# Performance work log

Measured on AMD Instinct MI355X. Metric: run time of the kernel, lower is better.

Reference implementation:

```python
import jax, jax.numpy as jnp
import numpy as np

N_NODES = 100000
IN_CH, HID_CH, OUT_CH = 128, 128, 64
N_EDGES = 1600000


def _gcn_conv(x, W, b, src, dst, num_nodes):
    """PyG GCNConv with gcn_norm(add_self_loops=True): adds one self-loop per
    node to the given edge set, symmetric deg^-1/2 normalization, then
    gather-scale-scatter of the linearly transformed features."""
    loop = jnp.arange(num_nodes)
    s = jnp.concatenate([src, loop])
    d = jnp.concatenate([dst, loop])
    # degree over targets (flow source_to_target), edge weights = 1
    deg = jax.ops.segment_sum(jnp.ones_like(s, x.dtype), d, num_segments=num_nodes)
    dinv = jnp.where(deg > 0, deg ** -0.5, 0.0)
    norm = dinv[s] * dinv[d]                      # [E']
    h = x @ W                                     # [N, out]
    msg = h[s] * norm[:, None]                    # [E', out] gather + scale
    out = jax.ops.segment_sum(msg, d, num_segments=num_nodes)  # scatter-add
    return out + b


def setup_inputs() -> dict:
    key = jax.random.key(0)
    k = jax.random.split(key, 6)
    x = jax.random.normal(k[0], (N_NODES, IN_CH), dtype=jnp.float32)
    edge_index = jax.random.randint(k[1], (2, N_EDGES), 0, N_NODES, dtype=jnp.int64)
    # Glorot-scale params
    W1 = jax.random.normal(k[2], (IN_CH, HID_CH), dtype=jnp.float32) * (2.0 / (IN_CH + HID_CH)) ** 0.5
    b1 = jnp.zeros((HID_CH,), dtype=jnp.float32)
    W2 = jax.random.normal(k[3], (HID_CH, OUT_CH), dtype=jnp.float32) * (2.0 / (HID_CH + OUT_CH)) ** 0.5
    b2 = jnp.zeros((OUT_CH,), dtype=jnp.float32)
    return {"x": x, "edge_index": edge_index, "W1": W1, "b1": b1, "W2": W2, "b2": b2}


def reference(x, edge_index, W1, b1, W2, b2):
    num_nodes = x.shape[0]
    loop = jnp.arange(num_nodes, dtype=edge_index.dtype)
    # wrapper-level add_self_loops (GCNConv adds another internally)
    src = jnp.concatenate([edge_index[0], loop])
    dst = jnp.concatenate([edge_index[1], loop])
    h = _gcn_conv(x, W1, b1, src, dst, num_nodes)
    h = jax.nn.relu(h)
    h = _gcn_conv(h, W2, b2, src, dst, num_nodes)
    return jax.nn.log_softmax(h, axis=1)
```

## Files before the change

### kernel.cpp

```cpp
#include <hip/hip_runtime.h>
#include <cstdint>
#include <cstddef>

#define IN_CH 128
#define HID_CH 128
#define OUT_CH 64
#define BSH 8
#define PB 4096

typedef unsigned int uint32;
typedef unsigned char uchar;
typedef short bf16x8 __attribute__((ext_vector_type(8)));
typedef float f32x4 __attribute__((ext_vector_type(4)));
typedef float f32x2 __attribute__((ext_vector_type(2)));

static __device__ __forceinline__ unsigned short f2bf(float f) {
    uint32 u = __float_as_uint(f);
    u += 0x7fffu + ((u >> 16) & 1u);
    return (unsigned short)(u >> 16);
}

typedef const __attribute__((address_space(1))) char gch;
typedef __attribute__((address_space(3))) char lch;
static __device__ __forceinline__ void gload16(const void* g, void* l) {
    __builtin_amdgcn_global_load_lds((gch*)g, (lch*)l, 16, 0, 0);
}


__global__ __launch_bounds__(256) void bhist_wtrans(
    const int* __restrict__ dst, int* __restrict__ bcnt, int E, int NB, int gP,
    const float* __restrict__ W1, const float* __restrict__ W2,
    unsigned short* __restrict__ W1t, unsigned short* __restrict__ W2t) {
    if (blockIdx.x >= (uint32)gP) {
        int t = (blockIdx.x - gP) * 256 + threadIdx.x;
        if (t < 128 * 128) {
            int nc = t >> 7, k = t & 127;
            W1t[t] = f2bf(W1[k * 128 + nc]);
        }
        int u = t - 128 * 128;
        if (u >= 0 && u < 64 * 128) {
            int nc = u >> 7, k = u & 127;
            W2t[u] = f2bf(W2[k * 64 + nc]);
        }
        return;
    }
    __shared__ int h[512];
    int t = threadIdx.x;
    int e0 = blockIdx.x * PB;
    int cnt = min(PB, E - e0);
    for (int b = t; b < NB; b += 256) h[b] = 0;
    __syncthreads();
    for (int i = t; i < cnt; i += 256)
        atomicAdd(&h[dst[e0 + i] >> BSH], 1);
    __syncthreads();
    for (int b = t; b < NB; b += 256)
        if (h[b]) atomicAdd(&bcnt[b], h[b]);
}

__global__ void bscan(const int* __restrict__ bcnt, int* __restrict__ bbase,
                      int* __restrict__ bcur, int NB, int E) {
    __shared__ int s[512];
    int t = threadIdx.x;
    int v = (t < NB) ? bcnt[t] : 0;
    s[t] = v;
    __syncthreads();
    for (int o = 1; o < 512; o <<= 1) {
        int add = (t >= o) ? s[t - o] : 0;
        __syncthreads();
        s[t] += add;
        __syncthreads();
    }
    if (t < NB) { bbase[t] = s[t] - v; bcur[t] = 0; }
    if (t == 0) bbase[NB] = E;
}

__global__ __launch_bounds__(256) void part1(
    const int* __restrict__ src, const int* __restrict__ dst,
    const int* __restrict__ bbase, int* __restrict__ bcur,
    int2* __restrict__ pairBuf, int E, int NB) {
    __shared__ int2 pairs[PB];
    __shared__ int hist[512];
    __shared__ int base[512];
    int t = threadIdx.x;
    int e0 = blockIdx.x * PB;
    int cnt = min(PB, E - e0);
    for (int b = t; b < NB; b += 256) hist[b] = 0;
    __syncthreads();
    for (int i = t; i < cnt; i += 256) {
        int s = src[e0 + i], d = dst[e0 + i];
        pairs[i] = make_int2(s, d);
        atomicAdd(&hist[d >> BSH], 1);
    }
    __syncthreads();
    for (int b = t; b < NB; b += 256) {
        int h = hist[b];
        int gb = (h > 0) ? atomicAdd(&bcur[b], h) : 0;
        base[b] = bbase[b] + gb;
        hist[b] = 0;
    }
    __syncthreads();
    for (int i = t; i < cnt; i += 256) {
        int2 p = pairs[i];
        int b = p.y >> BSH;
        int q = base[b] + atomicAdd(&hist[b], 1);
        pairBuf[q] = p;
    }
}

__global__ __launch_bounds__(256) void bucket_build(
    const int2* __restrict__ pairBuf, const int* __restrict__ bbase,
    int* __restrict__ rowptr, int* __restrict__ deg, float* __restrict__ dinv,
    int* __restrict__ csr, int N) {
    __shared__ int cnt[256];
    __shared__ int loc[256];
    int b = blockIdx.x, t = threadIdx.x;
    int start = bbase[b], end = bbase[b + 1];
    cnt[t] = 0;
    __syncthreads();
    for (int i = start + t; i < end; i += 256)
        atomicAdd(&cnt[pairBuf[i].y & 255], 1);
    __syncthreads();
    int v = cnt[t];
    loc[t] = v;
    __syncthreads();
    for (int o = 1; o < 256; o <<= 1) {
        int add = (t >= o) ? loc[t - o] : 0;
        __syncthreads();
        loc[t] += add;
        __syncthreads();
    }
    int excl = loc[t] - v;
    int node = (b << BSH) + t;
    if (node < N) {
        rowptr[node] = start + excl;
        deg[node] = v;
        dinv[node] = rsqrtf((float)(v + 2));
    }
    __syncthreads();
    cnt[t] = excl;
    __syncthreads();
    for (int i = start + t; i < end; i += 256) {
        int2 p = pairBuf[i];
        int q = start + atomicAdd(&cnt[p.y & 255], 1);
        csr[q] = p.x;
    }
}


__global__ __launch_bounds__(256) void gemm1_mfma(
    const float* __restrict__ A, const unsigned short* __restrict__ Wt,
    const float* __restrict__ dinv, uchar* __restrict__ C, int n, int nTiles) {
    constexpr int NT = 8;
    __shared__ unsigned short Ws[128 * 136];
    __shared__ char As[64 * 512];

    const int t = threadIdx.x;

    for (int i = t; i < 128 * 16; i += 256) {
        int rr = i >> 4, sq = i & 15;
        *(uint4*)&Ws[rr * 136 + sq * 8] = *(const uint4*)(Wt + rr * 128 + sq * 8);
    }

    const int w = t >> 6, l = t & 63;
    const int q = l >> 4, r16 = l & 15;
    const int rw = w * 16 + r16;

    for (int tile = blockIdx.x; tile < nTiles; tile += gridDim.x) {
        const int row0 = tile * 64;

#pragma unroll
        for (int rnd = 0; rnd < 8; rnd++) {
            int p = rnd * 4096 + t * 16;
            int row = row0 + (p >> 9);
            int col = p & 511;
            gload16((const char*)A + (size_t)min(row, n - 1) * 512 + col, As + p);
        }
        __syncthreads();

        f32x4 acc[NT];
#pragma unroll
        for (int i = 0; i < NT; i++) acc[i] = (f32x4){0.f, 0.f, 0.f, 0.f};

#pragma unroll
        for (int s = 0; s < 4; s++) {
            const int k0 = s * 32 + q * 8;
            const float* Arow = (const float*)(As + rw * 512);
            float4 v0 = *(const float4*)(Arow + k0);
            float4 v1 = *(const float4*)(Arow + k0 + 4);
            bf16x8 xf;
            xf[0] = (short)f2bf(v0.x); xf[1] = (short)f2bf(v0.y);
            xf[2] = (short)f2bf(v0.z); xf[3] = (short)f2bf(v0.w);
            xf[4] = (short)f2bf(v1.x); xf[5] = (short)f2bf(v1.y);
            xf[6] = (short)f2bf(v1.z); xf[7] = (short)f2bf(v1.w);
#pragma unroll
            for (int nt = 0; nt < NT; nt++) {
                bf16x8 wf = *(const bf16x8*)&Ws[(nt * 16 + r16) * 136 + k0];
                acc[nt] = __builtin_amdgcn_mfma_f32_16x16x32_bf16(wf, xf, acc[nt], 0, 0, 0);
            }
        }

        const int node = row0 + rw;
        const bool nv = node < n;
        const float dv = dinv[min(node, n - 1)];
        uchar* Crow = C + (size_t)node * 128;
#pragma unroll
        for (int nt = 0; nt < NT; nt++) {
            int pk = 0;
            pk = __builtin_amdgcn_cvt_pk_fp8_f32(acc[nt][0] * dv, acc[nt][1] * dv, pk, false);
            pk = __builtin_amdgcn_cvt_pk_fp8_f32(acc[nt][2] * dv, acc[nt][3] * dv, pk, true);
            if (nv) *(uint32*)(Crow + nt * 16 + q * 4) = (uint32)pk;
        }
        __syncthreads();
    }
}


__global__ __launch_bounds__(256) void agg1_fused(
    const uchar* __restrict__ H, const int* __restrict__ csr,
    const int* __restrict__ rowptr, const int* __restrict__ deg,
    const float* __restrict__ dinv, const float* __restrict__ bias,
    const unsigned short* __restrict__ W2t, uchar* __restrict__ H2, int n) {
    __shared__ unsigned short tile[16 * 136];
    int t = threadIdx.x;
    int g = t >> 4;
    int v = blockIdx.x * 16 + g;
    int hl = t & 15;
    int gsel = t & 48;
    bool valid = v < n;
    int vc = valid ? v : 0;
    int base = rowptr[vc];
    int cnt = valid ? deg[vc] : 0;
    const uint32 co = (uint32)(hl * 8);

    f32x2 A0 = (f32x2){0.f, 0.f}, A1 = A0, A2 = A0, A3 = A0;
    f32x2 B0 = A0, B1 = A0, B2 = A0, B3 = A0;

#define ACC128(h, s0, s1, s2, s3)                                   \
    {                                                               \
        s0 += __builtin_amdgcn_cvt_pk_f32_fp8((h).x, false);        \
        s1 += __builtin_amdgcn_cvt_pk_f32_fp8((h).x, true);         \
        s2 += __builtin_amdgcn_cvt_pk_f32_fp8((h).y, false);        \
        s3 += __builtin_amdgcn_cvt_pk_f32_fp8((h).y, true);         \
    }

    for (int j0 = 0; j0 < cnt; j0 += 16) {
        int nj = min(16, cnt - j0);
        int ul = 0;
        if (hl < nj) ul = csr[base + j0 + hl];
        int j = 0;
        for (; j + 8 <= nj; j += 8) {
            int u0 = __shfl(ul, (j + 0) | gsel), u1 = __shfl(ul, (j + 1) | gsel);
            int u2 = __shfl(ul, (j + 2) | gsel), u3 = __shfl(ul, (j + 3) | gsel);
            int u4 = __shfl(ul, (j + 4) | gsel), u5 = __shfl(ul, (j + 5) | gsel);
            int u6 = __shfl(ul, (j + 6) | gsel), u7 = __shfl(ul, (j + 7) | gsel);
            uint2 h0 = *(const uint2*)(H + (((uint32)u0 << 7) + co));
            uint2 h1 = *(const uint2*)(H + (((uint32)u1 << 7) + co));
            uint2 h2 = *(const uint2*)(H + (((uint32)u2 << 7) + co));
            uint2 h3 = *(const uint2*)(H + (((uint32)u3 << 7) + co));
            uint2 h4 = *(const uint2*)(H + (((uint32)u4 << 7) + co));
            uint2 h5 = *(const uint2*)(H + (((uint32)u5 << 7) + co));
            uint2 h6 = *(const uint2*)(H + (((uint32)u6 << 7) + co));
            uint2 h7 = *(const uint2*)(H + (((uint32)u7 << 7) + co));
            ACC128(h0, A0, A1, A2, A3);
            ACC128(h1, B0, B1, B2, B3);
            ACC128(h2, A0, A1, A2, A3);
            ACC128(h3, B0, B1, B2, B3);
            ACC128(h4, A0, A1, A2, A3);
            ACC128(h5, B0, B1, B2, B3);
            ACC128(h6, A0, A1, A2, A3);
            ACC128(h7, B0, B1, B2, B3);
        }
        for (; j + 4 <= nj; j += 4) {
            int u0 = __shfl(ul, (j + 0) | gsel), u1 = __shfl(ul, (j + 1) | gsel);
            int u2 = __shfl(ul, (j + 2) | gsel), u3 = __shfl(ul, (j + 3) | gsel);
            uint2 h0 = *(const uint2*)(H + (((uint32)u0 << 7) + co));
            uint2 h1 = *(const uint2*)(H + (((uint32)u1 << 7) + co));
            uint2 h2 = *(const uint2*)(H + (((uint32)u2 << 7) + co));
            uint2 h3 = *(const uint2*)(H + (((uint32)u3 << 7) + co));
            ACC128(h0, A0, A1, A2, A3);
            ACC128(h1, B0, B1, B2, B3);
            ACC128(h2, A0, A1, A2, A3);
            ACC128(h3, B0, B1, B2, B3);
        }
        for (; j < nj; j++) {
            int u = __shfl(ul, j | gsel);
            uint2 h = *(const uint2*)(H + (((uint32)u << 7) + co));
            ACC128(h, A0, A1, A2, A3);
        }
    }
#undef ACC128

    uint4 pk = make_uint4(0, 0, 0, 0);
    if (valid) {
        float dv = dinv[vc];
        uint2 hv = *(const uint2*)(H + (((uint32)vc << 7) + co));
        f32x2 s0 = __builtin_amdgcn_cvt_pk_f32_fp8(hv.x, false);
        f32x2 s1 = __builtin_amdgcn_cvt_pk_f32_fp8(hv.x, true);
        f32x2 s2 = __builtin_amdgcn_cvt_pk_f32_fp8(hv.y, false);
        f32x2 s3 = __builtin_amdgcn_cvt_pk_f32_fp8(hv.y, true);
        const f32x2* bp = (const f32x2*)(bias + hl * 8);
        f32x2 e0 = dv * ((A0 + B0) + 2.f * s0) + bp[0];
        f32x2 e1 = dv * ((A1 + B1) + 2.f * s1) + bp[1];
        f32x2 e2 = dv * ((A2 + B2) + 2.f * s2) + bp[2];
        f32x2 e3 = dv * ((A3 + B3) + 2.f * s3) + bp[3];
        float o0 = fmaxf(e0[0], 0.f), o1 = fmaxf(e0[1], 0.f);
        float o2 = fmaxf(e1[0], 0.f), o3 = fmaxf(e1[1], 0.f);
        float o4 = fmaxf(e2[0], 0.f), o5 = fmaxf(e2[1], 0.f);
        float o6 = fmaxf(e3[0], 0.f), o7 = fmaxf(e3[1], 0.f);
        pk.x = (uint32)f2bf(o0) | ((uint32)f2bf(o1) << 16);
        pk.y = (uint32)f2bf(o2) | ((uint32)f2bf(o3) << 16);
        pk.z = (uint32)f2bf(o4) | ((uint32)f2bf(o5) << 16);
        pk.w = (uint32)f2bf(o6) | ((uint32)f2bf(o7) << 16);
    }
    *(uint4*)&tile[g * 136 + hl * 8] = pk;
    __syncthreads();

    const int w = t >> 6, l = t & 63;
    const int q = l >> 4, r16 = l & 15;
    f32x4 acc2 = (f32x4){0.f, 0.f, 0.f, 0.f};
#pragma unroll
    for (int s = 0; s < 4; s++) {
        const int k0 = s * 32 + q * 8;
        bf16x8 hf = *(const bf16x8*)&tile[r16 * 136 + k0];
        bf16x8 wf = *(const bf16x8*)(W2t + (size_t)(w * 16 + r16) * 128 + k0);
        acc2 = __builtin_amdgcn_mfma_f32_16x16x32_bf16(wf, hf, acc2, 0, 0, 0);
    }
    const int node = blockIdx.x * 16 + r16;
    if (node < n) {
        const float dv2 = dinv[node];
        int pk2 = 0;
        pk2 = __builtin_amdgcn_cvt_pk_fp8_f32(acc2[0] * dv2, acc2[1] * dv2, pk2, false);
        pk2 = __builtin_amdgcn_cvt_pk_fp8_f32(acc2[2] * dv2, acc2[3] * dv2, pk2, true);
        *(uint32*)(H2 + (size_t)node * 64 + w * 16 + q * 4) = (uint32)pk2;
    }
}

__global__ __launch_bounds__(256) void agg_lsm_64(
    const uchar* __restrict__ H, const int* __restrict__ csr,
    const int* __restrict__ rowptr, const int* __restrict__ deg,
    const float* __restrict__ dinv, const float* __restrict__ bias,
    float* __restrict__ out, int n) {
    int v = blockIdx.x * 16 + (threadIdx.x >> 4);
    int hl = threadIdx.x & 15;
    int gsel = threadIdx.x & 48;
    bool valid = v < n;
    int vc = valid ? v : 0;
    int base = rowptr[vc];
    int cnt = valid ? deg[vc] : 0;
    const uint32 co = (uint32)(hl * 4);

    f32x2 A0 = (f32x2){0.f, 0.f}, A1 = A0, B0 = A0, B1 = A0;

#define ACC64(h, s0, s1)                                            \
    {                                                               \
        s0 += __builtin_amdgcn_cvt_pk_f32_fp8((h), false);          \
        s1 += __builtin_amdgcn_cvt_pk_f32_fp8((h), true);           \
    }

    for (int j0 = 0; j0 < cnt; j0 += 16) {
        int nj = min(16, cnt - j0);
        int ul = 0;
        if (hl < nj) ul = csr[base + j0 + hl];
        int j = 0;
        for (; j + 8 <= nj; j += 8) {
            int u0 = __shfl(ul, (j + 0) | gsel), u1 = __shfl(ul, (j + 1) | gsel);
            int u2 = __shfl(ul, (j + 2) | gsel), u3 = __shfl(ul, (j + 3) | gsel);
            int u4 = __shfl(ul, (j + 4) | gsel), u5 = __shfl(ul, (j + 5) | gsel);
            int u6 = __shfl(ul, (j + 6) | gsel), u7 = __shfl(ul, (j + 7) | gsel);
            uint32 h0 = *(const uint32*)(H + (((uint32)u0 << 6) + co));
            uint32 h1 = *(const uint32*)(H + (((uint32)u1 << 6) + co));
            uint32 h2 = *(const uint32*)(H + (((uint32)u2 << 6) + co));
            uint32 h3 = *(const uint32*)(H + (((uint32)u3 << 6) + co));
            uint32 h4 = *(const uint32*)(H + (((uint32)u4 << 6) + co));
            uint32 h5 = *(const uint32*)(H + (((uint32)u5 << 6) + co));
            uint32 h6 = *(const uint32*)(H + (((uint32)u6 << 6) + co));
            uint32 h7 = *(const uint32*)(H + (((uint32)u7 << 6) + co));
            ACC64(h0, A0, A1);
            ACC64(h1, B0, B1);
            ACC64(h2, A0, A1);
            ACC64(h3, B0, B1);
            ACC64(h4, A0, A1);
            ACC64(h5, B0, B1);
            ACC64(h6, A0, A1);
            ACC64(h7, B0, B1);
        }
        for (; j + 4 <= nj; j += 4) {
            int u0 = __shfl(ul, (j + 0) | gsel), u1 = __shfl(ul, (j + 1) | gsel);
            int u2 = __shfl(ul, (j + 2) | gsel), u3 = __shfl(ul, (j + 3) | gsel);
            uint32 h0 = *(const uint32*)(H + (((uint32)u0 << 6) + co));
            uint32 h1 = *(const uint32*)(H + (((uint32)u1 << 6) + co));
            uint32 h2 = *(const uint32*)(H + (((uint32)u2 << 6) + co));
            uint32 h3 = *(const uint32*)(H + (((uint32)u3 << 6) + co));
            ACC64(h0, A0, A1);
            ACC64(h1, B0, B1);
            ACC64(h2, A0, A1);
            ACC64(h3, B0, B1);
        }
        for (; j < nj; j++) {
            int u = __shfl(ul, j | gsel);
            uint32 h = *(const uint32*)(H + (((uint32)u << 6) + co));
            ACC64(h, A0, A1);
        }
    }
#undef ACC64

    float dv = dinv[vc];
    uint32 hv = *(const uint32*)(H + (((uint32)vc << 6) + co));
    f32x2 s0 = __builtin_amdgcn_cvt_pk_f32_fp8(hv, false);
    f32x2 s1 = __builtin_amdgcn_cvt_pk_f32_fp8(hv, true);
    const f32x2* bp = (const f32x2*)(bias + hl * 4);
    f32x2 w0 = dv * ((A0 + B0) + 2.f * s0) + bp[0];
    f32x2 w1 = dv * ((A1 + B1) + 2.f * s1) + bp[1];
    float v0 = w0[0], v1 = w0[1], v2 = w1[0], v3 = w1[1];
    float m = fmaxf(fmaxf(v0, v1), fmaxf(v2, v3));
    for (int o = 8; o > 0; o >>= 1) m = fmaxf(m, __shfl_xor(m, o));
    float e = (__expf(v0 - m) + __expf(v1 - m)) + (__expf(v2 - m) + __expf(v3 - m));
    for (int o = 8; o > 0; o >>= 1) e += __shfl_xor(e, o);
    float ls = m + __logf(e);
    if (valid)
        *(float4*)(out + (size_t)vc * 64 + hl * 4) =
            make_float4(v0 - ls, v1 - ls, v2 - ls, v3 - ls);
}


extern "C" void kernel_launch(void* const* d_in, const int* in_sizes, int n_in,
                              void* d_out, int out_size, void* d_ws, size_t ws_size,
                              hipStream_t stream) {
    const float* x  = (const float*)d_in[0];
    const int*   ei = (const int*)d_in[1];
    const float* W1 = (const float*)d_in[2];
    const float* b1 = (const float*)d_in[3];
    const float* W2 = (const float*)d_in[4];
    const float* b2 = (const float*)d_in[5];
    float* out = (float*)d_out;

    const int N = in_sizes[0] / IN_CH;
    const int E = in_sizes[1] / 2;
    const int* src = ei;
    const int* dst = ei + E;
    const int NB = (N + 255) >> BSH;

    char* w = (char*)d_ws;
    size_t off = 0;
    auto alloc = [&](size_t bytes) -> char* {
        char* p = w + off;
        off = (off + bytes + 255) & ~(size_t)255;
        return p;
    };
    int*   deg    = (int*)alloc((size_t)N * 4);
    int*   rowptr = (int*)alloc((size_t)N * 4);
    int*   bcnt   = (int*)alloc(512 * 4);
    int*   bbase  = (int*)alloc(513 * 4);
    int*   bcur   = (int*)alloc(512 * 4);
    float* dinv   = (float*)alloc((size_t)N * 4 + 1024);
    int*   csr    = (int*)alloc((size_t)E * 4);
    unsigned short* W1t = (unsigned short*)alloc(128 * 128 * 2);
    unsigned short* W2t = (unsigned short*)alloc(64 * 128 * 2);
    uchar* H1  = (uchar*)alloc((size_t)N * HID_CH);
    char*  scratch = alloc((size_t)E * 8);
    uchar* H2  = (uchar*)scratch;
    int2*  pairBuf = (int2*)scratch;

    hipMemsetAsync(bcnt, 0, 512 * 4, stream);

    int gP = (E + PB - 1) / PB;

    bhist_wtrans<<<gP + 96, 256, 0, stream>>>(dst, bcnt, E, NB, gP, W1, W2, W1t, W2t);
    bscan<<<1, 512, 0, stream>>>(bcnt, bbase, bcur, NB, E);
    part1<<<gP, 256, 0, stream>>>(src, dst, bbase, bcur, pairBuf, E, NB);
    bucket_build<<<NB, 256, 0, stream>>>(pairBuf, bbase, rowptr, deg, dinv, csr, N);

    const int nTiles = (N + 63) / 64;
    const int gG = min(nTiles, 512);
    gemm1_mfma<<<gG, 256, 0, stream>>>(x, W1t, dinv, H1, N, nTiles);
    agg1_fused<<<(N + 15) / 16, 256, 0, stream>>>(H1, csr, rowptr, deg, dinv, b1, W2t, H2, N);
    agg_lsm_64<<<(N + 15) / 16, 256, 0, stream>>>(H2, csr, rowptr, deg, dinv, b2, out, N);
}
```

Before: 242.4 us.

## Widen gather loads to 16 bytes and split neighbors across lane subgroups

Both aggregation kernels now gather 16-byte chunks of fp8 feature rows per lane instead of 8 or 4 bytes. The lanes of a node group are split into subgroups that process different neighbors in parallel, and the partial sums are combined with xor shuffles afterward. The first kernel also preloads its W2 fragments into registers before the gather loop. The goal is fewer, wider memory instructions for the latency-bound gather. The cost is extra shuffle reductions, more accumulator registers and a more complex tail handling.

```diff
diff --git a/kernel.cpp b/kernel.cpp
--- a/kernel.cpp
+++ b/kernel.cpp
@@ -230,17 +230,29 @@
     int vc = valid ? v : 0;
     int base = rowptr[vc];
     int cnt = valid ? deg[vc] : 0;
-    const uint32 co = (uint32)(hl * 8);
-
-    f32x2 A0 = (f32x2){0.f, 0.f}, A1 = A0, A2 = A0, A3 = A0;
-    f32x2 B0 = A0, B1 = A0, B2 = A0, B3 = A0;
-
-#define ACC128(h, s0, s1, s2, s3)                                   \
+    const int par = hl >> 3;
+    const uint32 co16 = (uint32)((hl & 7) * 16);
+
+    const int w = t >> 6, l = t & 63;
+    const int q = l >> 4, r16 = l & 15;
+    bf16x8 wf[4];
+#pragma unroll
+    for (int s = 0; s < 4; s++)
+        wf[s] = *(const bf16x8*)(W2t + (size_t)(w * 16 + r16) * 128 + s * 32 + q * 8);
+
+    f32x2 S0 = (f32x2){0.f, 0.f}, S1 = S0, S2 = S0, S3 = S0;
+    f32x2 S4 = S0, S5 = S0, S6 = S0, S7 = S0;
+
+#define ACCU4(h)                                                    \
     {                                                               \
-        s0 += __builtin_amdgcn_cvt_pk_f32_fp8((h).x, false);        \
-        s1 += __builtin_amdgcn_cvt_pk_f32_fp8((h).x, true);         \
-        s2 += __builtin_amdgcn_cvt_pk_f32_fp8((h).y, false);        \
-        s3 += __builtin_amdgcn_cvt_pk_f32_fp8((h).y, true);         \
+        S0 += __builtin_amdgcn_cvt_pk_f32_fp8((h).x, false);        \
+        S1 += __builtin_amdgcn_cvt_pk_f32_fp8((h).x, true);         \
+        S2 += __builtin_amdgcn_cvt_pk_f32_fp8((h).y, false);        \
+        S3 += __builtin_amdgcn_cvt_pk_f32_fp8((h).y, true);         \
+        S4 += __builtin_amdgcn_cvt_pk_f32_fp8((h).z, false);        \
+        S5 += __builtin_amdgcn_cvt_pk_f32_fp8((h).z, true);         \
+        S6 += __builtin_amdgcn_cvt_pk_f32_fp8((h).w, false);        \
+        S7 += __builtin_amdgcn_cvt_pk_f32_fp8((h).w, true);         \
     }
 
     for (int j0 = 0; j0 < cnt; j0 += 16) {
@@ -248,61 +260,60 @@
         int ul = 0;
         if (hl < nj) ul = csr[base + j0 + hl];
         int j = 0;
-        for (; j + 8 <= nj; j += 8) {
-            int u0 = __shfl(ul, (j + 0) | gsel), u1 = __shfl(ul, (j + 1) | gsel);
-            int u2 = __shfl(ul, (j + 2) | gsel), u3 = __shfl(ul, (j + 3) | gsel);
-            int u4 = __shfl(ul, (j + 4) | gsel), u5 = __shfl(ul, (j + 5) | gsel);
-            int u6 = __shfl(ul, (j + 6) | gsel), u7 = __shfl(ul, (j + 7) | gsel);
-            uint2 h0 = *(const uint2*)(H + (((uint32)u0 << 7) + co));
-            uint2 h1 = *(const uint2*)(H + (((uint32)u1 << 7) + co));
-            uint2 h2 = *(const uint2*)(H + (((uint32)u2 << 7) + co));
-            uint2 h3 = *(const uint2*)(H + (((uint32)u3 << 7) + co));
-            uint2 h4 = *(const uint2*)(H + (((uint32)u4 << 7) + co));
-            uint2 h5 = *(const uint2*)(H + (((uint32)u5 << 7) + co));
-            uint2 h6 = *(const uint2*)(H + (((uint32)u6 << 7) + co));
-            uint2 h7 = *(const uint2*)(H + (((uint32)u7 << 7) + co));
-            ACC128(h0, A0, A1, A2, A3);
-            ACC128(h1, B0, B1, B2, B3);
-            ACC128(h2, A0, A1, A2, A3);
-            ACC128(h3, B0, B1, B2, B3);
-            ACC128(h4, A0, A1, A2, A3);
-            ACC128(h5, B0, B1, B2, B3);
-            ACC128(h6, A0, A1, A2, A3);
-            ACC128(h7, B0, B1, B2, B3);
-        }
-        for (; j + 4 <= nj; j += 4) {
-            int u0 = __shfl(ul, (j + 0) | gsel), u1 = __shfl(ul, (j + 1) | gsel);
-            int u2 = __shfl(ul, (j + 2) | gsel), u3 = __shfl(ul, (j + 3) | gsel);
-            uint2 h0 = *(const uint2*)(H + (((uint32)u0 << 7) + co));
-            uint2 h1 = *(const uint2*)(H + (((uint32)u1 << 7) + co));
-            uint2 h2 = *(const uint2*)(H + (((uint32)u2 << 7) + co));
-            uint2 h3 = *(const uint2*)(H + (((uint32)u3 << 7) + co));
-            ACC128(h0, A0, A1, A2, A3);
-            ACC128(h1, B0, B1, B2, B3);
-            ACC128(h2, A0, A1, A2, A3);
-            ACC128(h3, B0, B1, B2, B3);
-        }
-        for (; j < nj; j++) {
+        for (; j + 16 <= nj; j += 16) {
+            int u0 = __shfl(ul, (j + 0 + par) | gsel);
+            int u1 = __shfl(ul, (j + 2 + par) | gsel);
+            int u2 = __shfl(ul, (j + 4 + par) | gsel);
+            int u3 = __shfl(ul, (j + 6 + par) | gsel);
+            int u4 = __shfl(ul, (j + 8 + par) | gsel);
+            int u5 = __shfl(ul, (j + 10 + par) | gsel);
+            int u6 = __shfl(ul, (j + 12 + par) | gsel);
+            int u7 = __shfl(ul, (j + 14 + par) | gsel);
+            uint4 h0 = *(const uint4*)(H + (((uint32)u0 << 7) + co16));
+            uint4 h1 = *(const uint4*)(H + (((uint32)u1 << 7) + co16));
+            uint4 h2 = *(const uint4*)(H + (((uint32)u2 << 7) + co16));
+            uint4 h3 = *(const uint4*)(H + (((uint32)u3 << 7) + co16));
+            uint4 h4 = *(const uint4*)(H + (((uint32)u4 << 7) + co16));
+            uint4 h5 = *(const uint4*)(H + (((uint32)u5 << 7) + co16));
+            uint4 h6 = *(const uint4*)(H + (((uint32)u6 << 7) + co16));
+            uint4 h7 = *(const uint4*)(H + (((uint32)u7 << 7) + co16));
+            ACCU4(h0); ACCU4(h1); ACCU4(h2); ACCU4(h3);
+            ACCU4(h4); ACCU4(h5); ACCU4(h6); ACCU4(h7);
+        }
+        for (; j + 2 <= nj; j += 2) {
+            int u = __shfl(ul, (j + par) | gsel);
+            uint4 h = *(const uint4*)(H + (((uint32)u << 7) + co16));
+            ACCU4(h);
+        }
+        if (j < nj) {
             int u = __shfl(ul, j | gsel);
-            uint2 h = *(const uint2*)(H + (((uint32)u << 7) + co));
-            ACC128(h, A0, A1, A2, A3);
-        }
-    }
-#undef ACC128
+            if (par == 0) {
+                uint4 h = *(const uint4*)(H + (((uint32)u << 7) + co16));
+                ACCU4(h);
+            }
+        }
+    }
+#undef ACCU4
+
+#define CMB8(S) { f32x2 T_; T_[0] = __shfl_xor(S[0], 8); T_[1] = __shfl_xor(S[1], 8); S += T_; }
+    CMB8(S0); CMB8(S1); CMB8(S2); CMB8(S3); CMB8(S4); CMB8(S5); CMB8(S6); CMB8(S7);
+#undef CMB8
 
     uint4 pk = make_uint4(0, 0, 0, 0);
     if (valid) {
         float dv = dinv[vc];
-        uint2 hv = *(const uint2*)(H + (((uint32)vc << 7) + co));
+        uint2 hv = *(const uint2*)(H + (((uint32)vc << 7) + co16 + (uint32)(par * 8)));
         f32x2 s0 = __builtin_amdgcn_cvt_pk_f32_fp8(hv.x, false);
         f32x2 s1 = __builtin_amdgcn_cvt_pk_f32_fp8(hv.x, true);
         f32x2 s2 = __builtin_amdgcn_cvt_pk_f32_fp8(hv.y, false);
         f32x2 s3 = __builtin_amdgcn_cvt_pk_f32_fp8(hv.y, true);
-        const f32x2* bp = (const f32x2*)(bias + hl * 8);
-        f32x2 e0 = dv * ((A0 + B0) + 2.f * s0) + bp[0];
-        f32x2 e1 = dv * ((A1 + B1) + 2.f * s1) + bp[1];
-        f32x2 e2 = dv * ((A2 + B2) + 2.f * s2) + bp[2];
-        f32x2 e3 = dv * ((A3 + B3) + 2.f * s3) + bp[3];
+        const f32x2* bp = (const f32x2*)(bias + (hl & 7) * 16 + par * 8);
+        f32x2 a0 = par ? S4 : S0, a1 = par ? S5 : S1;
+        f32x2 a2 = par ? S6 : S2, a3 = par ? S7 : S3;
+        f32x2 e0 = dv * (a0 + 2.f * s0) + bp[0];
+        f32x2 e1 = dv * (a1 + 2.f * s1) + bp[1];
+        f32x2 e2 = dv * (a2 + 2.f * s2) + bp[2];
+        f32x2 e3 = dv * (a3 + 2.f * s3) + bp[3];
         float o0 = fmaxf(e0[0], 0.f), o1 = fmaxf(e0[1], 0.f);
         float o2 = fmaxf(e1[0], 0.f), o3 = fmaxf(e1[1], 0.f);
         float o4 = fmaxf(e2[0], 0.f), o5 = fmaxf(e2[1], 0.f);
@@ -312,18 +323,14 @@
         pk.z = (uint32)f2bf(o4) | ((uint32)f2bf(o5) << 16);
         pk.w = (uint32)f2bf(o6) | ((uint32)f2bf(o7) << 16);
     }
-    *(uint4*)&tile[g * 136 + hl * 8] = pk;
-    __syncthreads();
-
-    const int w = t >> 6, l = t & 63;
-    const int q = l >> 4, r16 = l & 15;
+    *(uint4*)&tile[g * 136 + (hl & 7) * 16 + par * 8] = pk;
+    __syncthreads();
+
     f32x4 acc2 = (f32x4){0.f, 0.f, 0.f, 0.f};
 #pragma unroll
     for (int s = 0; s < 4; s++) {
-        const int k0 = s * 32 + q * 8;
-        bf16x8 hf = *(const bf16x8*)&tile[r16 * 136 + k0];
-        bf16x8 wf = *(const bf16x8*)(W2t + (size_t)(w * 16 + r16) * 128 + k0);
-        acc2 = __builtin_amdgcn_mfma_f32_16x16x32_bf16(wf, hf, acc2, 0, 0, 0);
+        bf16x8 hf = *(const bf16x8*)&tile[r16 * 136 + s * 32 + q * 8];
+        acc2 = __builtin_amdgcn_mfma_f32_16x16x32_bf16(wf[s], hf, acc2, 0, 0, 0);
     }
     const int node = blockIdx.x * 16 + r16;
     if (node < n) {
@@ -340,21 +347,30 @@
     const int* __restrict__ rowptr, const int* __restrict__ deg,
     const float* __restrict__ dinv, const float* __restrict__ bias,
     float* __restrict__ out, int n) {
-    int v = blockIdx.x * 16 + (threadIdx.x >> 4);
-    int hl = threadIdx.x & 15;
-    int gsel = threadIdx.x & 48;
+    int t = threadIdx.x;
+    int v = blockIdx.x * 16 + (t >> 4);
+    int hl = t & 15;
+    int gsel = t & 48;
     bool valid = v < n;
     int vc = valid ? v : 0;
     int base = rowptr[vc];
     int cnt = valid ? deg[vc] : 0;
-    const uint32 co = (uint32)(hl * 4);
-
-    f32x2 A0 = (f32x2){0.f, 0.f}, A1 = A0, B0 = A0, B1 = A0;
-
-#define ACC64(h, s0, s1)                                            \
+    const int par4 = hl >> 2;
+    const uint32 co16 = (uint32)((hl & 3) * 16);
+
+    f32x2 S0 = (f32x2){0.f, 0.f}, S1 = S0, S2 = S0, S3 = S0;
+    f32x2 S4 = S0, S5 = S0, S6 = S0, S7 = S0;
+
+#define ACCU4(h)                                                    \
     {                                                               \
-        s0 += __builtin_amdgcn_cvt_pk_f32_fp8((h), false);          \
-        s1 += __builtin_amdgcn_cvt_pk_f32_fp8((h), true);           \
+        S0 += __builtin_amdgcn_cvt_pk_f32_fp8((h).x, false);        \
+        S1 += __builtin_amdgcn_cvt_pk_f32_fp8((h).x, true);         \
+        S2 += __builtin_amdgcn_cvt_pk_f32_fp8((h).y, false);        \
+        S3 += __builtin_amdgcn_cvt_pk_f32_fp8((h).y, true);         \
+        S4 += __builtin_amdgcn_cvt_pk_f32_fp8((h).z, false);        \
+        S5 += __builtin_amdgcn_cvt_pk_f32_fp8((h).z, true);         \
+        S6 += __builtin_amdgcn_cvt_pk_f32_fp8((h).w, false);        \
+        S7 += __builtin_amdgcn_cvt_pk_f32_fp8((h).w, true);         \
     }
 
     for (int j0 = 0; j0 < cnt; j0 += 16) {
@@ -362,55 +378,51 @@
         int ul = 0;
         if (hl < nj) ul = csr[base + j0 + hl];
         int j = 0;
-        for (; j + 8 <= nj; j += 8) {
-            int u0 = __shfl(ul, (j + 0) | gsel), u1 = __shfl(ul, (j + 1) | gsel);
-            int u2 = __shfl(ul, (j + 2) | gsel), u3 = __shfl(ul, (j + 3) | gsel);
-            int u4 = __shfl(ul, (j + 4) | gsel), u5 = __shfl(ul, (j + 5) | gsel);
-            int u6 = __shfl(ul, (j + 6) | gsel), u7 = __shfl(ul, (j + 7) | gsel);
-            uint32 h0 = *(const uint32*)(H + (((uint32)u0 << 6) + co));
-            uint32 h1 = *(const uint32*)(H + (((uint32)u1 << 6) + co));
-            uint32 h2 = *(const uint32*)(H + (((uint32)u2 << 6) + co));
-            uint32 h3 = *(const uint32*)(H + (((uint32)u3 << 6) + co));
-            uint32 h4 = *(const uint32*)(H + (((uint32)u4 << 6) + co));
-            uint32 h5 = *(const uint32*)(H + (((uint32)u5 << 6) + co));
-            uint32 h6 = *(const uint32*)(H + (((uint32)u6 << 6) + co));
-            uint32 h7 = *(const uint32*)(H + (((uint32)u7 << 6) + co));
-            ACC64(h0, A0, A1);
-            ACC64(h1, B0, B1);
-            ACC64(h2, A0, A1);
-            ACC64(h3, B0, B1);
-            ACC64(h4, A0, A1);
-            ACC64(h5, B0, B1);
-            ACC64(h6, A0, A1);
-            ACC64(h7, B0, B1);
+        for (; j + 16 <= nj; j += 16) {
+            int u0 = __shfl(ul, (j + 0 + par4) | gsel);
+            int u1 = __shfl(ul, (j + 4 + par4) | gsel);
+            int u2 = __shfl(ul, (j + 8 + par4) | gsel);
+            int u3 = __shfl(ul, (j + 12 + par4) | gsel);
+            uint4 h0 = *(const uint4*)(H + (((uint32)u0 << 6) + co16));
+            uint4 h1 = *(const uint4*)(H + (((uint32)u1 << 6) + co16));
+            uint4 h2 = *(const uint4*)(H + (((uint32)u2 << 6) + co16));
+            uint4 h3 = *(const uint4*)(H + (((uint32)u3 << 6) + co16));
+            ACCU4(h0); ACCU4(h1); ACCU4(h2); ACCU4(h3);
         }
         for (; j + 4 <= nj; j += 4) {
-            int u0 = __shfl(ul, (j + 0) | gsel), u1 = __shfl(ul, (j + 1) | gsel);
-            int u2 = __shfl(ul, (j + 2) | gsel), u3 = __shfl(ul, (j + 3) | gsel);
-            uint32 h0 = *(const uint32*)(H + (((uint32)u0 << 6) + co));
-            uint32 h1 = *(const uint32*)(H + (((uint32)u1 << 6) + co));
-            uint32 h2 = *(const uint32*)(H + (((uint32)u2 << 6) + co));
-            uint32 h3 = *(const uint32*)(H + (((uint32)u3 << 6) + co));
-            ACC64(h0, A0, A1);
-            ACC64(h1, B0, B1);
-            ACC64(h2, A0, A1);
-            ACC64(h3, B0, B1);
-        }
-        for (; j < nj; j++) {
-            int u = __shfl(ul, j | gsel);
-            uint32 h = *(const uint32*)(H + (((uint32)u << 6) + co));
-            ACC64(h, A0, A1);
-        }
-    }
-#undef ACC64
+            int u = __shfl(ul, (j + par4) | gsel);
+            uint4 h = *(const uint4*)(H + (((uint32)u << 6) + co16));
+            ACCU4(h);
+        }
+        int rem = nj - j;
+        if (rem) {
+            int u = __shfl(ul, ((j + par4) & 15) | gsel);
+            if (par4 < rem) {
+                uint4 h = *(const uint4*)(H + (((uint32)u << 6) + co16));
+                ACCU4(h);
+            }
+        }
+    }
+#undef ACCU4
+
+#define CMB(S, M) { f32x2 T_; T_[0] = __shfl_xor(S[0], M); T_[1] = __shfl_xor(S[1], M); S += T_; }
+    CMB(S0, 4); CMB(S1, 4); CMB(S2, 4); CMB(S3, 4);
+    CMB(S4, 4); CMB(S5, 4); CMB(S6, 4); CMB(S7, 4);
+    CMB(S0, 8); CMB(S1, 8); CMB(S2, 8); CMB(S3, 8);
+    CMB(S4, 8); CMB(S5, 8); CMB(S6, 8); CMB(S7, 8);
+#undef CMB
+
+    f32x2 a0 = (par4 == 0) ? S0 : (par4 == 1) ? S2 : (par4 == 2) ? S4 : S6;
+    f32x2 a1 = (par4 == 0) ? S1 : (par4 == 1) ? S3 : (par4 == 2) ? S5 : S7;
+    const uint32 off = co16 + (uint32)(par4 * 4);
 
     float dv = dinv[vc];
-    uint32 hv = *(const uint32*)(H + (((uint32)vc << 6) + co));
+    uint32 hv = *(const uint32*)(H + (((uint32)vc << 6) + off));
     f32x2 s0 = __builtin_amdgcn_cvt_pk_f32_fp8(hv, false);
     f32x2 s1 = __builtin_amdgcn_cvt_pk_f32_fp8(hv, true);
-    const f32x2* bp = (const f32x2*)(bias + hl * 4);
-    f32x2 w0 = dv * ((A0 + B0) + 2.f * s0) + bp[0];
-    f32x2 w1 = dv * ((A1 + B1) + 2.f * s1) + bp[1];
+    const f32x2* bp = (const f32x2*)(bias + off);
+    f32x2 w0 = dv * (a0 + 2.f * s0) + bp[0];
+    f32x2 w1 = dv * (a1 + 2.f * s1) + bp[1];
     float v0 = w0[0], v1 = w0[1], v2 = w1[0], v3 = w1[1];
     float m = fmaxf(fmaxf(v0, v1), fmaxf(v2, v3));
     for (int o = 8; o > 0; o >>= 1) m = fmaxf(m, __shfl_xor(m, o));
@@ -418,7 +430,7 @@
     for (int o = 8; o > 0; o >>= 1) e += __shfl_xor(e, o);
     float ls = m + __logf(e);
     if (valid)
-        *(float4*)(out + (size_t)vc * 64 + hl * 4) =
+        *(float4*)(out + (size_t)vc * 64 + off) =
             make_float4(v0 - ls, v1 - ls, v2 - ls, v3 - ls);
 }
 
```

Measured after the change: 263.7 us. 1.09x slower.

## Stage neighbor row gathers through LDS with direct 16-byte global-to-LDS loads

Applied to the files above, without the earlier changes.

Both aggregation kernels now fetch neighbor feature rows with 16-byte direct global-to-LDS loads (gload16) into a per-wave staging buffer. Each lane then reads its slice back from LDS and accumulates. The aim is wider, more coalesced gather transactions and fewer small per-lane global loads. In exchange it adds LDS usage (32KB and 16KB per block), which may cut occupancy. It also waits on all loads per 16-edge chunk and always issues loads for 16 edges, even when fewer are valid.

```diff
diff --git a/kernel.cpp b/kernel.cpp
--- a/kernel.cpp
+++ b/kernel.cpp
@@ -220,17 +220,19 @@
     const int* __restrict__ rowptr, const int* __restrict__ deg,
     const float* __restrict__ dinv, const float* __restrict__ bias,
     const unsigned short* __restrict__ W2t, uchar* __restrict__ H2, int n) {
+    __shared__ char stage[4][8192];
     __shared__ unsigned short tile[16 * 136];
     int t = threadIdx.x;
-    int g = t >> 4;
-    int v = blockIdx.x * 16 + g;
+    int slot = t >> 4;
+    int v = blockIdx.x * 16 + slot;
     int hl = t & 15;
     int gsel = t & 48;
+    int w = t >> 6;
+    int gg = (t >> 4) & 3;
     bool valid = v < n;
     int vc = valid ? v : 0;
     int base = rowptr[vc];
     int cnt = valid ? deg[vc] : 0;
-    const uint32 co = (uint32)(hl * 8);
 
     f32x2 A0 = (f32x2){0.f, 0.f}, A1 = A0, A2 = A0, A3 = A0;
     f32x2 B0 = A0, B1 = A0, B2 = A0, B3 = A0;
@@ -243,53 +245,34 @@
         s3 += __builtin_amdgcn_cvt_pk_f32_fp8((h).y, true);         \
     }
 
+    char* sl = stage[w];
+    const char* rg = sl + gg * 256 + hl * 8;
+
     for (int j0 = 0; j0 < cnt; j0 += 16) {
         int nj = min(16, cnt - j0);
         int ul = 0;
         if (hl < nj) ul = csr[base + j0 + hl];
-        int j = 0;
-        for (; j + 8 <= nj; j += 8) {
-            int u0 = __shfl(ul, (j + 0) | gsel), u1 = __shfl(ul, (j + 1) | gsel);
-            int u2 = __shfl(ul, (j + 2) | gsel), u3 = __shfl(ul, (j + 3) | gsel);
-            int u4 = __shfl(ul, (j + 4) | gsel), u5 = __shfl(ul, (j + 5) | gsel);
-            int u6 = __shfl(ul, (j + 6) | gsel), u7 = __shfl(ul, (j + 7) | gsel);
-            uint2 h0 = *(const uint2*)(H + (((uint32)u0 << 7) + co));
-            uint2 h1 = *(const uint2*)(H + (((uint32)u1 << 7) + co));
-            uint2 h2 = *(const uint2*)(H + (((uint32)u2 << 7) + co));
-            uint2 h3 = *(const uint2*)(H + (((uint32)u3 << 7) + co));
-            uint2 h4 = *(const uint2*)(H + (((uint32)u4 << 7) + co));
-            uint2 h5 = *(const uint2*)(H + (((uint32)u5 << 7) + co));
-            uint2 h6 = *(const uint2*)(H + (((uint32)u6 << 7) + co));
-            uint2 h7 = *(const uint2*)(H + (((uint32)u7 << 7) + co));
-            ACC128(h0, A0, A1, A2, A3);
-            ACC128(h1, B0, B1, B2, B3);
-            ACC128(h2, A0, A1, A2, A3);
-            ACC128(h3, B0, B1, B2, B3);
-            ACC128(h4, A0, A1, A2, A3);
-            ACC128(h5, B0, B1, B2, B3);
-            ACC128(h6, A0, A1, A2, A3);
-            ACC128(h7, B0, B1, B2, B3);
-        }
-        for (; j + 4 <= nj; j += 4) {
-            int u0 = __shfl(ul, (j + 0) | gsel), u1 = __shfl(ul, (j + 1) | gsel);
-            int u2 = __shfl(ul, (j + 2) | gsel), u3 = __shfl(ul, (j + 3) | gsel);
-            uint2 h0 = *(const uint2*)(H + (((uint32)u0 << 7) + co));
-            uint2 h1 = *(const uint2*)(H + (((uint32)u1 << 7) + co));
-            uint2 h2 = *(const uint2*)(H + (((uint32)u2 << 7) + co));
-            uint2 h3 = *(const uint2*)(H + (((uint32)u3 << 7) + co));
-            ACC128(h0, A0, A1, A2, A3);
-            ACC128(h1, B0, B1, B2, B3);
-            ACC128(h2, A0, A1, A2, A3);
-            ACC128(h3, B0, B1, B2, B3);
-        }
-        for (; j < nj; j++) {
+#pragma unroll
+        for (int i = 0; i < 8; i++) {
+            int j = i * 2 + (hl >> 3);
             int u = __shfl(ul, j | gsel);
-            uint2 h = *(const uint2*)(H + (((uint32)u << 7) + co));
-            ACC128(h, A0, A1, A2, A3);
+            gload16(H + (((uint32)u << 7) + ((uint32)(hl & 7) << 4)),
+                    sl + i * 1024);
+        }
+        asm volatile("s_waitcnt vmcnt(0)" ::: "memory");
+        __builtin_amdgcn_sched_barrier(0);
+#pragma unroll
+        for (int j = 0; j < 16; j++) {
+            if (j < nj) {
+                uint2 h = *(const uint2*)(rg + (j >> 1) * 1024 + (j & 1) * 128);
+                if (j & 1) { ACC128(h, B0, B1, B2, B3); }
+                else       { ACC128(h, A0, A1, A2, A3); }
+            }
         }
     }
 #undef ACC128
 
+    const uint32 co = (uint32)(hl * 8);
     uint4 pk = make_uint4(0, 0, 0, 0);
     if (valid) {
         float dv = dinv[vc];
@@ -312,10 +295,10 @@
         pk.z = (uint32)f2bf(o4) | ((uint32)f2bf(o5) << 16);
         pk.w = (uint32)f2bf(o6) | ((uint32)f2bf(o7) << 16);
     }
-    *(uint4*)&tile[g * 136 + hl * 8] = pk;
-    __syncthreads();
-
-    const int w = t >> 6, l = t & 63;
+    *(uint4*)&tile[slot * 136 + hl * 8] = pk;
+    __syncthreads();
+
+    const int l = t & 63;
     const int q = l >> 4, r16 = l & 15;
     f32x4 acc2 = (f32x4){0.f, 0.f, 0.f, 0.f};
 #pragma unroll
@@ -340,9 +323,13 @@
     const int* __restrict__ rowptr, const int* __restrict__ deg,
     const float* __restrict__ dinv, const float* __restrict__ bias,
     float* __restrict__ out, int n) {
-    int v = blockIdx.x * 16 + (threadIdx.x >> 4);
-    int hl = threadIdx.x & 15;
-    int gsel = threadIdx.x & 48;
+    __shared__ char stage[4][4096];
+    int t = threadIdx.x;
+    int v = blockIdx.x * 16 + (t >> 4);
+    int hl = t & 15;
+    int gsel = t & 48;
+    int w = t >> 6;
+    int gg = (t >> 4) & 3;
     bool valid = v < n;
     int vc = valid ? v : 0;
     int base = rowptr[vc];
@@ -357,49 +344,29 @@
         s1 += __builtin_amdgcn_cvt_pk_f32_fp8((h), true);           \
     }
 
+    char* sl = stage[w];
+    const char* rg = sl + gg * 256 + hl * 4;
+
     for (int j0 = 0; j0 < cnt; j0 += 16) {
         int nj = min(16, cnt - j0);
         int ul = 0;
         if (hl < nj) ul = csr[base + j0 + hl];
-        int j = 0;
-        for (; j + 8 <= nj; j += 8) {
-            int u0 = __shfl(ul, (j + 0) | gsel), u1 = __shfl(ul, (j + 1) | gsel);
-            int u2 = __shfl(ul, (j + 2) | gsel), u3 = __shfl(ul, (j + 3) | gsel);
-            int u4 = __shfl(ul, (j + 4) | gsel), u5 = __shfl(ul, (j + 5) | gsel);
-            int u6 = __shfl(ul, (j + 6) | gsel), u7 = __shfl(ul, (j + 7) | gsel);
-            uint32 h0 = *(const uint32*)(H + (((uint32)u0 << 6) + co));
-            uint32 h1 = *(const uint32*)(H + (((uint32)u1 << 6) + co));
-            uint32 h2 = *(const uint32*)(H + (((uint32)u2 << 6) + co));
-            uint32 h3 = *(const uint32*)(H + (((uint32)u3 << 6) + co));
-            uint32 h4 = *(const uint32*)(H + (((uint32)u4 << 6) + co));
-            uint32 h5 = *(const uint32*)(H + (((uint32)u5 << 6) + co));
-            uint32 h6 = *(const uint32*)(H + (((uint32)u6 << 6) + co));
-            uint32 h7 = *(const uint32*)(H + (((uint32)u7 << 6) + co));
-            ACC64(h0, A0, A1);
-            ACC64(h1, B0, B1);
-            ACC64(h2, A0, A1);
-            ACC64(h3, B0, B1);
-            ACC64(h4, A0, A1);
-            ACC64(h5, B0, B1);
-            ACC64(h6, A0, A1);
-            ACC64(h7, B0, B1);
-        }
-        for (; j + 4 <= nj; j += 4) {
-            int u0 = __shfl(ul, (j + 0) | gsel), u1 = __shfl(ul, (j + 1) | gsel);
-            int u2 = __shfl(ul, (j + 2) | gsel), u3 = __shfl(ul, (j + 3) | gsel);
-            uint32 h0 = *(const uint32*)(H + (((uint32)u0 << 6) + co));
-            uint32 h1 = *(const uint32*)(H + (((uint32)u1 << 6) + co));
-            uint32 h2 = *(const uint32*)(H + (((uint32)u2 << 6) + co));
-            uint32 h3 = *(const uint32*)(H + (((uint32)u3 << 6) + co));
-            ACC64(h0, A0, A1);
-            ACC64(h1, B0, B1);
-            ACC64(h2, A0, A1);
-            ACC64(h3, B0, B1);
-        }
-        for (; j < nj; j++) {
+#pragma unroll
+        for (int i = 0; i < 4; i++) {
+            int j = i * 4 + (hl >> 2);
             int u = __shfl(ul, j | gsel);
-            uint32 h = *(const uint32*)(H + (((uint32)u << 6) + co));
-            ACC64(h, A0, A1);
+            gload16(H + (((uint32)u << 6) + ((uint32)(hl & 3) << 4)),
+                    sl + i * 1024);
+        }
+        asm volatile("s_waitcnt vmcnt(0)" ::: "memory");
+        __builtin_amdgcn_sched_barrier(0);
+#pragma unroll
+        for (int j = 0; j < 16; j++) {
+            if (j < nj) {
+                uint32 h = *(const uint32*)(rg + (j >> 2) * 1024 + (j & 3) * 64);
+                if (j & 1) { ACC64(h, B0, B1); }
+                else       { ACC64(h, A0, A1); }
+            }
         }
     }
 #undef ACC64
```

Result: faster. 234.0 us (-3.5%).
